# Optimization experiments

Hardware: AMD Instinct MI355X
Metric: run time of the kernel (lower is better)

## Reference

```python
import jax, jax.numpy as jnp
import numpy as np

B, D_IN, H, D_OUT = 4096, 4096, 2048, 1000
LN_EPS = 1e-5


def setup_inputs() -> dict:
    key = jax.random.key(0)
    ks = jax.random.split(key, 8)
    s_in = 1.0 / np.sqrt(H)  # torch RNN init: U(-1/sqrt(H), 1/sqrt(H))
    inp = {
        "x": jax.random.normal(ks[0], (B, D_IN), dtype=jnp.float32),
        "W_ih0": jax.random.uniform(ks[1], (H, D_IN), jnp.float32, -s_in, s_in),
        "b_ih0": jax.random.uniform(ks[2], (H,), jnp.float32, -s_in, s_in),
        "b_hh0": jax.random.uniform(ks[3], (H,), jnp.float32, -s_in, s_in),
        "W_ih1": jax.random.uniform(ks[4], (H, H), jnp.float32, -s_in, s_in),
        "b_ih1": jax.random.uniform(ks[5], (H,), jnp.float32, -s_in, s_in),
        "b_hh1": jax.random.uniform(ks[6], (H,), jnp.float32, -s_in, s_in),
        "ln_g": jnp.ones((2 * H,), jnp.float32),
        "ln_b": jnp.zeros((2 * H,), jnp.float32),
        "fc_W": jax.random.uniform(ks[7], (D_OUT, 2 * H), jnp.float32, -1.0 / np.sqrt(2 * H), 1.0 / np.sqrt(2 * H)),
        "fc_b": jnp.zeros((D_OUT,), jnp.float32),
    }
    return inp


def reference(x, W_ih0, b_ih0, b_hh0, W_ih1, b_ih1, b_hh1, ln_g, ln_b, fc_W, fc_b):
    # seq_len == 1, h0 == 0 -> W_hh terms vanish; only biases remain.
    h1 = jnp.tanh(x @ W_ih0.T + b_ih0 + b_hh0)          # [B, H]
    h2 = jnp.tanh(h1 @ W_ih1.T + b_ih1 + b_hh1)         # [B, H]
    # last_hidden == mean_pooled (single step) -> concat duplicates h2
    combined = jnp.concatenate([h2, h2], axis=1)        # [B, 2H]
    mu = combined.mean(axis=-1, keepdims=True)
    var = combined.var(axis=-1, keepdims=True)
    normed = (combined - mu) * jax.lax.rsqrt(var + LN_EPS) * ln_g + ln_b
    # dropout is identity in eval mode
    return normed @ fc_W.T + fc_b                        # [B, D_OUT]
```

## Files before the change

### kernel.cpp

```cpp
#include <hip/hip_runtime.h>
#include <hip/hip_bf16.h>

typedef __attribute__((ext_vector_type(8))) unsigned short ushort8;
typedef __attribute__((ext_vector_type(8))) __bf16 bf16x8;
typedef __attribute__((ext_vector_type(4))) float f32x4;
typedef __attribute__((ext_vector_type(4))) float floatx4;

__device__ __forceinline__ unsigned short f2bf(float f) {
    unsigned u = __builtin_bit_cast(unsigned, f);
    u += 0x7fffu + ((u >> 16) & 1u);
    return (unsigned short)(u >> 16);
}
__device__ __forceinline__ float bf2f(unsigned short h) {
    unsigned u = ((unsigned)h) << 16;
    return __builtin_bit_cast(float, u);
}

__device__ __forceinline__ void gload_lds16(const void* g, void* l) {
    __builtin_amdgcn_global_load_lds(
        (const __attribute__((address_space(1))) void*)g,
        (__attribute__((address_space(3))) void*)l,
        16, 0, 0);
}

#define BAR()   asm volatile("s_barrier" ::: "memory")
#define VMW(n)  asm volatile("s_waitcnt vmcnt(" #n ")" ::: "memory")
#define LGK(n)  asm volatile("s_waitcnt lgkmcnt(" #n ")" ::: "memory")

__global__ __launch_bounds__(256) void cvt_f2bf(const float* __restrict__ in,
                                                unsigned short* __restrict__ out,
                                                int n8) {
    int i = blockIdx.x * 256 + threadIdx.x;
    if (i >= n8) return;
    floatx4 a = ((const floatx4*)in)[2 * i];
    floatx4 b = ((const floatx4*)in)[2 * i + 1];
    ushort8 o;
#pragma unroll
    for (int j = 0; j < 4; ++j) { o[j] = f2bf(a[j]); o[4 + j] = f2bf(b[j]); }
    ((ushort8*)out)[i] = o;
}

__global__ __launch_bounds__(256) void weff_kernel(const float* __restrict__ fcW,
                                                   const float* __restrict__ lng,
                                                   const float* __restrict__ lnb,
                                                   const float* __restrict__ fcb,
                                                   unsigned short* __restrict__ weff,
                                                   float* __restrict__ cc,
                                                   float* __restrict__ wsum) {
    int o = blockIdx.x;
    int tid = threadIdx.x;
    if (o >= 1000) {
        ushort8 z = {0, 0, 0, 0, 0, 0, 0, 0};
        ((ushort8*)(weff + (size_t)o * 2048))[tid] = z;
        if (tid == 0) { cc[o] = 0.f; wsum[o] = 0.f; }
        return;
    }
    const float* wrow = fcW + (size_t)o * 4096;
    int j0 = tid * 8;
    floatx4 wa  = *(const floatx4*)(wrow + j0);
    floatx4 wb  = *(const floatx4*)(wrow + j0 + 4);
    floatx4 wa2 = *(const floatx4*)(wrow + 2048 + j0);
    floatx4 wb2 = *(const floatx4*)(wrow + 2048 + j0 + 4);
    floatx4 ga  = *(const floatx4*)(lng + j0);
    floatx4 gb  = *(const floatx4*)(lng + j0 + 4);
    floatx4 ga2 = *(const floatx4*)(lng + 2048 + j0);
    floatx4 gb2 = *(const floatx4*)(lng + 2048 + j0 + 4);
    floatx4 ba  = *(const floatx4*)(lnb + j0);
    floatx4 bb  = *(const floatx4*)(lnb + j0 + 4);
    floatx4 ba2 = *(const floatx4*)(lnb + 2048 + j0);
    floatx4 bb2 = *(const floatx4*)(lnb + 2048 + j0 + 4);
    ushort8 o8;
    float acc = 0.f, ws = 0.f;
#pragma unroll
    for (int j = 0; j < 4; ++j) {
        o8[j] = f2bf(ga[j] * wa[j] + ga2[j] * wa2[j]);
        acc += ba[j] * wa[j] + ba2[j] * wa2[j];
        ws  += bf2f(o8[j]);
        o8[4 + j] = f2bf(gb[j] * wb[j] + gb2[j] * wb2[j]);
        acc += bb[j] * wb[j] + bb2[j] * wb2[j];
        ws  += bf2f(o8[4 + j]);
    }
    ((ushort8*)(weff + (size_t)o * 2048))[tid] = o8;
#pragma unroll
    for (int d = 32; d; d >>= 1) { acc += __shfl_down(acc, d); ws += __shfl_down(ws, d); }
    __shared__ float red[4], redw[4];
    if ((tid & 63) == 0) { red[tid >> 6] = acc; redw[tid >> 6] = ws; }
    __syncthreads();
    if (tid == 0) {
        cc[o] = fcb[o] + red[0] + red[1] + red[2] + red[3];
        wsum[o] = redw[0] + redw[1] + redw[2] + redw[3];
    }
}

__global__ __launch_bounds__(256) void ln_stats(const unsigned short* __restrict__ h2,
                                                float2* __restrict__ mur) {
    int row = blockIdx.x, tid = threadIdx.x;
    ushort8 v = ((const ushort8*)(h2 + (size_t)row * 2048))[tid];
    float s = 0.f, s2 = 0.f;
#pragma unroll
    for (int j = 0; j < 8; ++j) { float f = bf2f(v[j]); s += f; s2 += f * f; }
#pragma unroll
    for (int d = 32; d; d >>= 1) { s += __shfl_down(s, d); s2 += __shfl_down(s2, d); }
    __shared__ float rs_[4], rs2_[4];
    if ((tid & 63) == 0) { rs_[tid >> 6] = s; rs2_[tid >> 6] = s2; }
    __syncthreads();
    if (tid == 0) {
        float S = rs_[0] + rs_[1] + rs_[2] + rs_[3];
        float S2 = rs2_[0] + rs2_[1] + rs2_[2] + rs2_[3];
        float mu = S * (1.f / 2048.f);
        float var = S2 * (1.f / 2048.f) - mu * mu;
        mur[row] = make_float2(mu, rsqrtf(var + 1e-5f));
    }
}

template <int EPI, int NJ>
__global__ __launch_bounds__(512, 2) void gemm_p2(const unsigned short* __restrict__ A,
                                                  const unsigned short* __restrict__ B,
                                                  int M, int N, int K,
                                                  const float* __restrict__ bias0,
                                                  const float* __restrict__ bias1,
                                                  void* __restrict__ Cout, int ncols,
                                                  const float2* __restrict__ mur,
                                                  const float* __restrict__ wsum) {
    extern __shared__ char smem[];
    constexpr int BUFSZ = 8192 + NJ * 4096;
    const int tid = threadIdx.x;
    const int lane = tid & 63, wid = tid >> 6;
    const int wm = wid >> 2, wn = wid & 3;
    const int fr = lane & 15, g = lane >> 4;

    const int nwg = gridDim.x * gridDim.y;
    const int fid = blockIdx.y * gridDim.x + blockIdx.x;
    const int cpx = nwg >> 3;
    const int sw = (fid & 7) * cpx + (fid >> 3);
    const int bx = sw % gridDim.x, by = sw / gridDim.x;
    const int row0 = by * 128, col0 = bx * (64 * NJ);

    const int srow = tid >> 2;
    const int scole = (((tid & 3) << 4) ^ ((srow & 3) << 4)) >> 1;

    auto stage = [&](int kt, char* buf) {
        gload_lds16(A + (size_t)(row0 + srow) * K + kt * 32 + scole, buf + tid * 16);
#pragma unroll
        for (int rr = 0; rr < NJ / 2; ++rr)
            gload_lds16(B + (size_t)(col0 + rr * 128 + srow) * K + kt * 32 + scole,
                        buf + 8192 + rr * 8192 + tid * 16);
    };

    const int kbyte = (g * 16) ^ ((fr & 3) << 4);
    auto readFrags = [&](bf16x8 (&fa)[4], bf16x8 (&fb)[NJ], const char* buf) {
#pragma unroll
        for (int m = 0; m < 4; ++m)
            fa[m] = __builtin_bit_cast(bf16x8,
                *(const ushort8*)(buf + (wm * 64 + m * 16 + fr) * 64 + kbyte));
#pragma unroll
        for (int n = 0; n < NJ; ++n)
            fb[n] = __builtin_bit_cast(bf16x8,
                *(const ushort8*)(buf + 8192 + (wn * (16 * NJ) + n * 16 + fr) * 64 + kbyte));
    };

    f32x4 acc[4][NJ];
#pragma unroll
    for (int i = 0; i < 4; ++i)
#pragma unroll
        for (int j = 0; j < NJ; ++j) acc[i][j] = f32x4{0.f, 0.f, 0.f, 0.f};

    auto domfma = [&](bf16x8 (&fa)[4], bf16x8 (&fb)[NJ]) {
        __builtin_amdgcn_s_setprio(1);
#pragma unroll
        for (int m = 0; m < 4; ++m)
#pragma unroll
            for (int n = 0; n < NJ; ++n)
                acc[m][n] = __builtin_amdgcn_mfma_f32_16x16x32_bf16(fa[m], fb[n], acc[m][n], 0, 0, 0);
        __builtin_amdgcn_s_setprio(0);
    };

    auto waitL = [&]() { if constexpr (NJ == 4) VMW(3); else VMW(2); };
    auto guard = [&]() { if constexpr (NJ == 4) LGK(8); else LGK(6); };

    char* q0 = smem;
    char* q1 = smem + BUFSZ;
    char* q2 = smem + 2 * BUFSZ;
    char* q3 = smem + 3 * BUFSZ;

    bf16x8 faA[4], fbA[NJ], faB[4], fbB[NJ];

    stage(0, q0); stage(1, q1); stage(2, q2);
    if constexpr (NJ == 4) VMW(6); else VMW(4);
    BAR();
    readFrags(faA, fbA, q0);

    const int NT = K >> 5;
    for (int t = 0; t < NT; t += 2) {
        if (t + 2 < NT) waitL(); else VMW(0);
        guard();
        BAR();
        if (t + 3 < NT) stage(t + 3, q3);
        readFrags(faB, fbB, q1);
        domfma(faA, fbA);
        { char* tmp = q0; q0 = q1; q1 = q2; q2 = q3; q3 = tmp; }

        if (t + 3 < NT) waitL(); else VMW(0);
        guard();
        BAR();
        if (t + 4 < NT) stage(t + 4, q3);
        if (t + 2 < NT) readFrags(faA, fbA, q1);
        domfma(faB, fbB);
        { char* tmp = q0; q0 = q1; q1 = q2; q2 = q3; q3 = tmp; }
    }

#pragma unroll
    for (int i = 0; i < 4; ++i) {
        int rbase = row0 + wm * 64 + i * 16 + g * 4;
        if (EPI == 0) {
#pragma unroll
            for (int j = 0; j < NJ; ++j) {
                int col = col0 + wn * (16 * NJ) + j * 16 + fr;
                float bsum = bias0[col] + bias1[col];
                unsigned short* O = (unsigned short*)Cout;
#pragma unroll
                for (int r = 0; r < 4; ++r)
                    O[(size_t)(rbase + r) * N + col] = f2bf(tanhf(acc[i][j][r] + bsum));
            }
        } else {
            float2 mr[4];
#pragma unroll
            for (int r = 0; r < 4; ++r) mr[r] = mur[rbase + r];
#pragma unroll
            for (int j = 0; j < NJ; ++j) {
                int col = col0 + wn * (16 * NJ) + j * 16 + fr;
                if (col < ncols) {
                    float ws = wsum[col];
                    float ccv = bias0[col];
                    float* O = (float*)Cout;
#pragma unroll
                    for (int r = 0; r < 4; ++r)
                        O[(size_t)(rbase + r) * ncols + col] =
                            mr[r].y * (acc[i][j][r] - mr[r].x * ws) + ccv;
                }
            }
        }
    }
}

extern "C" void kernel_launch(void* const* d_in, const int* in_sizes, int n_in,
                              void* d_out, int out_size, void* d_ws, size_t ws_size,
                              hipStream_t stream) {
    const float* x   = (const float*)d_in[0];
    const float* W0  = (const float*)d_in[1];
    const float* bi0 = (const float*)d_in[2];
    const float* bh0 = (const float*)d_in[3];
    const float* W1  = (const float*)d_in[4];
    const float* bi1 = (const float*)d_in[5];
    const float* bh1 = (const float*)d_in[6];
    const float* lng = (const float*)d_in[7];
    const float* lnb = (const float*)d_in[8];
    const float* fcW = (const float*)d_in[9];
    const float* fcb = (const float*)d_in[10];
    float* out = (float*)d_out;

    char* w = (char*)d_ws;
    unsigned short* xb   = (unsigned short*)(w);
    unsigned short* w0b  = (unsigned short*)(w + 33554432ull);
    unsigned short* w1b  = (unsigned short*)(w + 50331648ull);
    unsigned short* h1   = (unsigned short*)(w + 58720256ull);
    unsigned short* h2   = (unsigned short*)(w + 75497472ull);
    unsigned short* weff = (unsigned short*)(w + 92274688ull);
    float* cc            = (float*)(w + 96468992ull);
    float* wsum          = (float*)(w + 96473088ull);
    float2* mur          = (float2*)(w + 96477184ull);

    const int SHM0 = 4 * (8192 + 4 * 4096);
    const int SHM1 = 4 * (8192 + 2 * 4096);
    (void)hipFuncSetAttribute((const void*)gemm_p2<0, 4>,
                              hipFuncAttributeMaxDynamicSharedMemorySize, SHM0);
    (void)hipFuncSetAttribute((const void*)gemm_p2<1, 2>,
                              hipFuncAttributeMaxDynamicSharedMemorySize, SHM1);

    cvt_f2bf<<<8192, 256, 0, stream>>>(x,  xb,  2097152);
    cvt_f2bf<<<4096, 256, 0, stream>>>(W0, w0b, 1048576);
    cvt_f2bf<<<2048, 256, 0, stream>>>(W1, w1b, 524288);
    weff_kernel<<<1024, 256, 0, stream>>>(fcW, lng, lnb, fcb, weff, cc, wsum);
    gemm_p2<0, 4><<<dim3(8, 32), 512, SHM0, stream>>>(xb, w0b, 4096, 2048, 4096,
                                                      bi0, bh0, h1, 2048, nullptr, nullptr);
    gemm_p2<0, 4><<<dim3(8, 32), 512, SHM0, stream>>>(h1, w1b, 4096, 2048, 2048,
                                                      bi1, bh1, h2, 2048, nullptr, nullptr);
    ln_stats<<<4096, 256, 0, stream>>>(h2, mur);
    gemm_p2<1, 2><<<dim3(8, 32), 512, SHM1, stream>>>(h2, weff, 4096, 1024, 2048,
                                                      cc, nullptr, out, 1000, mur, wsum);
}
```

Before: 194.4 us.

## Double K-tile depth to 64 and switch GEMM to 3-buffer LDS ring

The GEMM main loop now stages 64-wide K tiles instead of 32, with a 3-bit XOR swizzle on 128-byte LDS rows, and issues two MFMAs per fragment pair per tile. The 4-slot rotating buffer with lgkmcnt guards becomes a 3-slot ring indexed modulo 3, with the prefetch issued before the wait and barrier. This halves the number of barriers and iterations per K, at the cost of more LDS per block (144KB or 96KB), which may lower occupancy, and a shallower prefetch distance.

```diff
diff --git a/kernel.cpp b/kernel.cpp
--- a/kernel.cpp
+++ b/kernel.cpp
@@ -25,7 +25,6 @@
 
 #define BAR()   asm volatile("s_barrier" ::: "memory")
 #define VMW(n)  asm volatile("s_waitcnt vmcnt(" #n ")" ::: "memory")
-#define LGK(n)  asm volatile("s_waitcnt lgkmcnt(" #n ")" ::: "memory")
 
 __global__ __launch_bounds__(256) void cvt_f2bf(const float* __restrict__ in,
                                                 unsigned short* __restrict__ out,
@@ -114,7 +113,7 @@
 }
 
 template <int EPI, int NJ>
-__global__ __launch_bounds__(512, 2) void gemm_p2(const unsigned short* __restrict__ A,
+__global__ __launch_bounds__(512, 2) void gemm_rp(const unsigned short* __restrict__ A,
                                                   const unsigned short* __restrict__ B,
                                                   int M, int N, int K,
                                                   const float* __restrict__ bias0,
@@ -123,7 +122,7 @@
                                                   const float2* __restrict__ mur,
                                                   const float* __restrict__ wsum) {
     extern __shared__ char smem[];
-    constexpr int BUFSZ = 8192 + NJ * 4096;
+    constexpr int BUFSZ = 16384 + NJ * 8192;
     const int tid = threadIdx.x;
     const int lane = tid & 63, wid = tid >> 6;
     const int wm = wid >> 2, wn = wid & 3;
@@ -136,27 +135,34 @@
     const int bx = sw % gridDim.x, by = sw / gridDim.x;
     const int row0 = by * 128, col0 = bx * (64 * NJ);
 
-    const int srow = tid >> 2;
-    const int scole = (((tid & 3) << 4) ^ ((srow & 3) << 4)) >> 1;
+    const int tg = tid >> 3;
+    const int tcE = ((tid & 7) ^ (tg & 7)) * 8;
 
     auto stage = [&](int kt, char* buf) {
-        gload_lds16(A + (size_t)(row0 + srow) * K + kt * 32 + scole, buf + tid * 16);
-#pragma unroll
-        for (int rr = 0; rr < NJ / 2; ++rr)
-            gload_lds16(B + (size_t)(col0 + rr * 128 + srow) * K + kt * 32 + scole,
-                        buf + 8192 + rr * 8192 + tid * 16);
+#pragma unroll
+        for (int r = 0; r < 2; ++r)
+            gload_lds16(A + (size_t)(row0 + r * 64 + tg) * K + kt * 64 + tcE,
+                        buf + r * 8192 + wid * 1024);
+#pragma unroll
+        for (int rr = 0; rr < NJ; ++rr)
+            gload_lds16(B + (size_t)(col0 + rr * 64 + tg) * K + kt * 64 + tcE,
+                        buf + 16384 + rr * 8192 + wid * 1024);
     };
 
-    const int kbyte = (g * 16) ^ ((fr & 3) << 4);
-    auto readFrags = [&](bf16x8 (&fa)[4], bf16x8 (&fb)[NJ], const char* buf) {
+    const int xorv = (fr & 7) << 4;
+    auto readFrags = [&](bf16x8 (&fa)[4][2], bf16x8 (&fb)[NJ][2], const char* buf) {
 #pragma unroll
         for (int m = 0; m < 4; ++m)
-            fa[m] = __builtin_bit_cast(bf16x8,
-                *(const ushort8*)(buf + (wm * 64 + m * 16 + fr) * 64 + kbyte));
+#pragma unroll
+            for (int kh = 0; kh < 2; ++kh)
+                fa[m][kh] = __builtin_bit_cast(bf16x8, *(const ushort8*)(
+                    buf + (wm * 64 + m * 16 + fr) * 128 + ((kh * 64 + g * 16) ^ xorv)));
 #pragma unroll
         for (int n = 0; n < NJ; ++n)
-            fb[n] = __builtin_bit_cast(bf16x8,
-                *(const ushort8*)(buf + 8192 + (wn * (16 * NJ) + n * 16 + fr) * 64 + kbyte));
+#pragma unroll
+            for (int kh = 0; kh < 2; ++kh)
+                fb[n][kh] = __builtin_bit_cast(bf16x8, *(const ushort8*)(
+                    buf + 16384 + (wn * (16 * NJ) + n * 16 + fr) * 128 + ((kh * 64 + g * 16) ^ xorv)));
     };
 
     f32x4 acc[4][NJ];
@@ -165,48 +171,48 @@
 #pragma unroll
         for (int j = 0; j < NJ; ++j) acc[i][j] = f32x4{0.f, 0.f, 0.f, 0.f};
 
-    auto domfma = [&](bf16x8 (&fa)[4], bf16x8 (&fb)[NJ]) {
+    auto domfma = [&](bf16x8 (&fa)[4][2], bf16x8 (&fb)[NJ][2]) {
         __builtin_amdgcn_s_setprio(1);
 #pragma unroll
         for (int m = 0; m < 4; ++m)
 #pragma unroll
             for (int n = 0; n < NJ; ++n)
-                acc[m][n] = __builtin_amdgcn_mfma_f32_16x16x32_bf16(fa[m], fb[n], acc[m][n], 0, 0, 0);
+#pragma unroll
+                for (int kh = 0; kh < 2; ++kh)
+                    acc[m][n] = __builtin_amdgcn_mfma_f32_16x16x32_bf16(fa[m][kh], fb[n][kh], acc[m][n], 0, 0, 0);
         __builtin_amdgcn_s_setprio(0);
     };
 
-    auto waitL = [&]() { if constexpr (NJ == 4) VMW(3); else VMW(2); };
-    auto guard = [&]() { if constexpr (NJ == 4) LGK(8); else LGK(6); };
-
-    char* q0 = smem;
-    char* q1 = smem + BUFSZ;
-    char* q2 = smem + 2 * BUFSZ;
-    char* q3 = smem + 3 * BUFSZ;
-
-    bf16x8 faA[4], fbA[NJ], faB[4], fbB[NJ];
-
-    stage(0, q0); stage(1, q1); stage(2, q2);
+    bf16x8 aX[4][2], bX[NJ][2], aY[4][2], bY[NJ][2];
+
+    stage(0, smem); stage(1, smem + BUFSZ);
     if constexpr (NJ == 4) VMW(6); else VMW(4);
     BAR();
-    readFrags(faA, fbA, q0);
-
-    const int NT = K >> 5;
+    readFrags(aX, bX, smem);
+
+    const int NT = K >> 6;
     for (int t = 0; t < NT; t += 2) {
-        if (t + 2 < NT) waitL(); else VMW(0);
-        guard();
+        if (t + 2 < NT) {
+            stage(t + 2, smem + ((t + 2) % 3) * BUFSZ);
+            if constexpr (NJ == 4) VMW(6); else VMW(4);
+        } else {
+            VMW(0);
+        }
         BAR();
-        if (t + 3 < NT) stage(t + 3, q3);
-        readFrags(faB, fbB, q1);
-        domfma(faA, fbA);
-        { char* tmp = q0; q0 = q1; q1 = q2; q2 = q3; q3 = tmp; }
-
-        if (t + 3 < NT) waitL(); else VMW(0);
-        guard();
-        BAR();
-        if (t + 4 < NT) stage(t + 4, q3);
-        if (t + 2 < NT) readFrags(faA, fbA, q1);
-        domfma(faB, fbB);
-        { char* tmp = q0; q0 = q1; q1 = q2; q2 = q3; q3 = tmp; }
+        readFrags(aY, bY, smem + ((t + 1) % 3) * BUFSZ);
+        domfma(aX, bX);
+
+        if (t + 2 < NT) {
+            if (t + 3 < NT) {
+                stage(t + 3, smem + ((t + 3) % 3) * BUFSZ);
+                if constexpr (NJ == 4) VMW(6); else VMW(4);
+            } else {
+                VMW(0);
+            }
+            BAR();
+            readFrags(aX, bX, smem + ((t + 2) % 3) * BUFSZ);
+        }
+        domfma(aY, bY);
     }
 
 #pragma unroll
@@ -270,22 +276,22 @@
     float* wsum          = (float*)(w + 96473088ull);
     float2* mur          = (float2*)(w + 96477184ull);
 
-    const int SHM0 = 4 * (8192 + 4 * 4096);
-    const int SHM1 = 4 * (8192 + 2 * 4096);
-    (void)hipFuncSetAttribute((const void*)gemm_p2<0, 4>,
+    const int SHM0 = 3 * (16384 + 4 * 8192);
+    const int SHM1 = 3 * (16384 + 2 * 8192);
+    (void)hipFuncSetAttribute((const void*)gemm_rp<0, 4>,
                               hipFuncAttributeMaxDynamicSharedMemorySize, SHM0);
-    (void)hipFuncSetAttribute((const void*)gemm_p2<1, 2>,
+    (void)hipFuncSetAttribute((const void*)gemm_rp<1, 2>,
                               hipFuncAttributeMaxDynamicSharedMemorySize, SHM1);
 
     cvt_f2bf<<<8192, 256, 0, stream>>>(x,  xb,  2097152);
     cvt_f2bf<<<4096, 256, 0, stream>>>(W0, w0b, 1048576);
     cvt_f2bf<<<2048, 256, 0, stream>>>(W1, w1b, 524288);
     weff_kernel<<<1024, 256, 0, stream>>>(fcW, lng, lnb, fcb, weff, cc, wsum);
-    gemm_p2<0, 4><<<dim3(8, 32), 512, SHM0, stream>>>(xb, w0b, 4096, 2048, 4096,
+    gemm_rp<0, 4><<<dim3(8, 32), 512, SHM0, stream>>>(xb, w0b, 4096, 2048, 4096,
                                                       bi0, bh0, h1, 2048, nullptr, nullptr);
-    gemm_p2<0, 4><<<dim3(8, 32), 512, SHM0, stream>>>(h1, w1b, 4096, 2048, 2048,
+    gemm_rp<0, 4><<<dim3(8, 32), 512, SHM0, stream>>>(h1, w1b, 4096, 2048, 2048,
                                                       bi1, bh1, h2, 2048, nullptr, nullptr);
     ln_stats<<<4096, 256, 0, stream>>>(h2, mur);
-    gemm_p2<1, 2><<<dim3(8, 32), 512, SHM1, stream>>>(h2, weff, 4096, 1024, 2048,
+    gemm_rp<1, 2><<<dim3(8, 32), 512, SHM1, stream>>>(h2, weff, 4096, 1024, 2048,
                                                       cc, nullptr, out, 1000, mur, wsum);
 }
```

Result: faster. 174.8 us (-10.1%).
